# Optimization experiments

Measured on AMD Instinct MI355X. Metric: run time of the kernel, lower is better.

Reference implementation:

```python
import jax, jax.numpy as jnp
import numpy as np

B = 16      # number of point clouds
N = 4096    # points per cloud (max after densify)
D = 3       # xyz


def setup_inputs() -> dict:
    key = jax.random.key(0)
    k1, k2 = jax.random.split(key)
    pred = jax.random.normal(k1, (B * N, D), dtype=jnp.float32)
    target = jax.random.normal(k2, (B * N, D), dtype=jnp.float32)
    # sorted segment ids, equal-sized clouds (faithful to to_dense_batch usage)
    batch = jnp.repeat(jnp.arange(B, dtype=jnp.int64), N)
    return {"pred": pred, "target": target, "batch": batch}


def to_dense_batch(x, batch, num_batches, max_n):
    # PyG to_dense_batch: scatter flat points into [B, max_n, D], zero-padded.
    ones = jnp.ones_like(batch)
    counts = jax.ops.segment_sum(ones, batch, num_segments=num_batches)
    offsets = jnp.concatenate([jnp.zeros((1,), batch.dtype), jnp.cumsum(counts)[:-1]])
    pos = jnp.arange(batch.shape[0], dtype=batch.dtype) - offsets[batch]
    dense = jnp.zeros((num_batches, max_n, x.shape[-1]), x.dtype)
    return dense.at[batch, pos].set(x)


def chamfer_distance(x, y):
    # squared-euclidean pairwise distances via the GEMM identity
    x2 = jnp.sum(x * x, axis=-1)                      # [B, N]
    y2 = jnp.sum(y * y, axis=-1)                      # [B, M]
    xy = jnp.einsum('bnd,bmd->bnm', x, y)             # [B, N, M]
    d = x2[:, :, None] + y2[:, None, :] - 2.0 * xy    # [B, N, M]
    cham_x = jnp.mean(jnp.min(d, axis=2), axis=1)     # mean over N of min over M
    cham_y = jnp.mean(jnp.min(d, axis=1), axis=1)     # mean over M of min over N
    # point_reduction='mean', batch_reduction='mean' (pytorch3d defaults)
    return jnp.mean(cham_x + cham_y)


def reference(pred, target, batch):
    x = to_dense_batch(pred, batch, B, N)
    y = to_dense_batch(target, batch, B, N)
    return chamfer_distance(x, y)
```

## Files before the change

kernel.cpp:

```cpp
#include <hip/hip_runtime.h>


namespace {

constexpr int kB = 16;
constexpr int kN = 4096;
constexpr int kPlane = kB * kN;
constexpr int kStage = 512;
constexpr int kNS = kN / kStage;
constexpr float kScale = 1.0f / (float)(kB * kN);

typedef short bf16x8 __attribute__((ext_vector_type(8)));
typedef float f32x16 __attribute__((ext_vector_type(16)));
typedef unsigned short u16;

__device__ inline u16 bf16_rn(float f) {
  union { float f; unsigned u; } v; v.f = f;
  unsigned r = v.u + 0x7fffu + ((v.u >> 16) & 1u);
  return (u16)(r >> 16);
}
__device__ inline float bf16_f(u16 h) {
  union { unsigned u; float f; } v; v.u = (unsigned)h << 16;
  return v.f;
}
__device__ inline unsigned pk2(u16 lo, u16 hi) {
  return (unsigned)lo | ((unsigned)hi << 16);
}

__global__ void init_out(float* out) { out[0] = 0.0f; }

__global__ __launch_bounds__(256) void cd_prep(
    const float* __restrict__ pred, const float* __restrict__ targ,
    u16* __restrict__ Apred, u16* __restrict__ Atarg,
    u16* __restrict__ Bpred, u16* __restrict__ Btarg,
    float* __restrict__ out) {
  const int p = blockIdx.x * 256 + threadIdx.x;
  if (p == 0) out[0] = 0.0f;
  const int cloud = p >> 12, q = p & (kN - 1);
  const int stg = q >> 9, pl = q & (kStage - 1);
  const size_t boff = (size_t)cloud * 65536 + (size_t)stg * 8192 + (size_t)pl * 8;
  const u16 one = 0x3F80;

  const float* srcs[2] = {pred, targ};
  u16* adsts[2] = {Apred, Atarg};
  u16* bdsts[2] = {Bpred, Btarg};
#pragma unroll
  for (int which = 0; which < 2; ++which) {
    const float a = srcs[which][3 * p], c = srcs[which][3 * p + 1],
                d = srcs[which][3 * p + 2];
    const u16 ah = bf16_rn(a), ch = bf16_rn(c), dh = bf16_rn(d);
    const u16 al = bf16_rn(a - bf16_f(ah));
    const u16 cl = bf16_rn(c - bf16_f(ch));
    const u16 dl = bf16_rn(d - bf16_f(dh));
    const float s2 = fmaf(a, a, fmaf(c, c, d * d));
    const u16 s2h = bf16_rn(s2);
    const u16 s2l = bf16_rn(s2 - bf16_f(s2h));
    {
      uint4 w0, w1;
      w0.x = pk2(ah, ch); w0.y = pk2(dh, al); w0.z = pk2(cl, dl); w0.w = pk2(ah, ch);
      w1.x = pk2(dh, s2h); w1.y = pk2(s2l, one); w1.z = pk2(one, al); w1.w = pk2(cl, dl);
      uint4* dst = reinterpret_cast<uint4*>(adsts[which] + (size_t)p * 16);
      dst[0] = w0; dst[1] = w1;
    }
    {
      const u16 nah = bf16_rn(-2.0f * bf16_f(ah));
      const u16 nch = bf16_rn(-2.0f * bf16_f(ch));
      const u16 ndh = bf16_rn(-2.0f * bf16_f(dh));
      const u16 nal = bf16_rn(-2.0f * bf16_f(al));
      const u16 ncl = bf16_rn(-2.0f * bf16_f(cl));
      const u16 ndl = bf16_rn(-2.0f * bf16_f(dl));
      uint4 w0, w1;
      w0.x = pk2(nah, nch); w0.y = pk2(ndh, nah); w0.z = pk2(nch, ndh); w0.w = pk2(nal, ncl);
      w1.x = pk2(ndl, one); w1.y = pk2(one, s2h); w1.z = pk2(s2l, nal); w1.w = pk2(ncl, ndl);
      *reinterpret_cast<uint4*>(bdsts[which] + boff) = w0;
      *reinterpret_cast<uint4*>(bdsts[which] + boff + 4096) = w1;
    }
  }
}

__global__ __launch_bounds__(256) void cd_mfma(
    const u16* __restrict__ Apred, const u16* __restrict__ Atarg,
    const u16* __restrict__ Bpred, const u16* __restrict__ Btarg,
    float* __restrict__ out) {
  __shared__ uint4 Blds4[2048];
  __shared__ float wsum[4];

  const int t = threadIdx.x;
  const int w = t >> 6, lane = t & 63;
  const int half = lane >> 5, l31 = lane & 31;
  const int chunk = blockIdx.x;
  const int cloud = blockIdx.y;
  const int dir = blockIdx.z;
  const u16* __restrict__ A = dir ? Atarg : Apred;
  const u16* __restrict__ B = dir ? Bpred : Btarg;

  const int arow = cloud * kN + chunk * 128 + w * 32 + l31;
  union { uint4 u; bf16x8 v; } afu;
  afu.u = *reinterpret_cast<const uint4*>(A + (size_t)arow * 16 + half * 8);
  const bf16x8 afrag = afu.v;

  const char* bcloud = (const char*)B + (size_t)cloud * 131072;
  char* ldsbase = (char*)Blds4;
#define STAGE(st, buf)                                                        \
  {                                                                           \
    const char* _src = bcloud + (size_t)(st) * 16384;                         \
    char* _dst = ldsbase + (buf) * 16384;                                     \
    _Pragma("unroll")                                                         \
    for (int i = 0; i < 4; ++i) {                                             \
      __builtin_amdgcn_global_load_lds(                                       \
          (const __attribute__((address_space(1))) void*)(_src +              \
              ((w * 4 + i) * 64 + lane) * 16),                                \
          (__attribute__((address_space(3))) void*)(_dst + (w * 4 + i) * 1024),\
          16, 0, 0);                                                          \
    }                                                                         \
  }

  f32x16 zacc;
#pragma unroll
  for (int r = 0; r < 16; ++r) zacc[r] = 0.0f;
  float rmin[16];
#pragma unroll
  for (int r = 0; r < 16; ++r) rmin[r] = 1e30f;

  STAGE(0, 0);
  __syncthreads();

  for (int st = 0; st < kNS; ++st) {
    if (st < kNS - 1) STAGE(st + 1, (st + 1) & 1);
    const char* blc = ldsbase + (st & 1) * 16384 + half * 8192 + l31 * 16;
#pragma unroll
    for (int jt = 0; jt < kStage / 64; ++jt) {
      union { uint4 u; bf16x8 v; } B0, B1;
      B0.u = *reinterpret_cast<const uint4*>(blc + jt * 1024);
      B1.u = *reinterpret_cast<const uint4*>(blc + jt * 1024 + 512);
      const f32x16 s0 =
          __builtin_amdgcn_mfma_f32_32x32x16_bf16(afrag, B0.v, zacc, 0, 0, 0);
      const f32x16 s1 =
          __builtin_amdgcn_mfma_f32_32x32x16_bf16(afrag, B1.v, zacc, 0, 0, 0);
#pragma unroll
      for (int r = 0; r < 16; ++r)
        asm("v_min3_f32 %0, %0, %1, %2"
            : "+v"(rmin[r]) : "v"(s0[r]), "v"(s1[r]));
    }
    __syncthreads();
  }
#undef STAGE

#pragma unroll
  for (int st = 1; st < 32; st <<= 1) {
#pragma unroll
    for (int r = 0; r < 16; ++r)
      rmin[r] = fminf(rmin[r], __shfl_xor(rmin[r], st, 64));
  }
  float s = 0.0f;
#pragma unroll
  for (int r = 0; r < 16; ++r) s += rmin[r];
  s = (l31 == 0) ? s : 0.0f;
  s += __shfl_down(s, 32, 64);
  if (lane == 0) wsum[w] = s;
  __syncthreads();
  if (t == 0)
    atomicAdd(out, (wsum[0] + wsum[1] + wsum[2] + wsum[3]) * kScale);
}

template <int KX>
__global__ __launch_bounds__(256) void chamfer_direct(
    const float* __restrict__ pred, const float* __restrict__ targ,
    float* __restrict__ out) {
  __shared__ float4 tA[128], tB[128];
  const int t = threadIdx.x;
  const int xb = blockIdx.x, b = blockIdx.y, dir = blockIdx.z;
  const float* __restrict__ X = dir ? targ : pred;
  const float* __restrict__ Y = dir ? pred : targ;
  float2 xx2[KX], xy2[KX], xz2[KX];
  float x2[KX], mn[KX];
  const int ibase = b * kN + xb * (256 * KX) + t;
#pragma unroll
  for (int k = 0; k < KX; ++k) {
    const int i = ibase + k * 256;
    const float a = X[3 * i], c = X[3 * i + 1], d = X[3 * i + 2];
    x2[k] = fmaf(a, a, fmaf(c, c, d * d));
    xx2[k] = make_float2(-2.0f * a, -2.0f * a);
    xy2[k] = make_float2(-2.0f * c, -2.0f * c);
    xz2[k] = make_float2(-2.0f * d, -2.0f * d);
    mn[k] = 1e30f;
  }
  for (int t0 = 0; t0 < kN; t0 += 256) {
    __syncthreads();
    if (t < 128) {
      const int j0 = 3 * (b * kN + t0 + 2 * t);
      const float a0 = Y[j0], c0 = Y[j0 + 1], d0 = Y[j0 + 2];
      const float a1 = Y[j0 + 3], c1 = Y[j0 + 4], d1 = Y[j0 + 5];
      tA[t] = make_float4(a0, a1, c0, c1);
      tB[t] = make_float4(d0, d1, fmaf(a0, a0, fmaf(c0, c0, d0 * d0)),
                          fmaf(a1, a1, fmaf(c1, c1, d1 * d1)));
    }
    __syncthreads();
    for (int jj = 0; jj < 128; ++jj) {
      const float4 qa = tA[jj], qb = tB[jj];
      const float2 qx = make_float2(qa.x, qa.y), qy = make_float2(qa.z, qa.w);
      const float2 qz = make_float2(qb.x, qb.y), qw = make_float2(qb.z, qb.w);
#pragma unroll
      for (int k = 0; k < KX; ++k) {
        float2 acc;
        asm("v_pk_fma_f32 %0, %1, %2, %3\n\t"
            "v_pk_fma_f32 %0, %4, %5, %0\n\t"
            "v_pk_fma_f32 %0, %6, %7, %0"
            : "=&v"(acc)
            : "v"(xz2[k]), "v"(qz), "v"(qw), "v"(xy2[k]), "v"(qy),
              "v"(xx2[k]), "v"(qx));
        asm("v_min3_f32 %0, %0, %1, %2" : "+v"(mn[k]) : "v"(acc.x), "v"(acc.y));
      }
    }
  }
  float s = 0.0f;
#pragma unroll
  for (int k = 0; k < KX; ++k) s += x2[k] + mn[k];
  for (int o = 32; o > 0; o >>= 1) s += __shfl_down(s, o, 64);
  __shared__ float wsum[4];
  const int lane = t & 63, wv = t >> 6;
  if (lane == 0) wsum[wv] = s;
  __syncthreads();
  if (t == 0)
    atomicAdd(out, (wsum[0] + wsum[1] + wsum[2] + wsum[3]) * kScale);
}

}

extern "C" void kernel_launch(void* const* d_in, const int* in_sizes, int n_in,
                              void* d_out, int out_size, void* d_ws,
                              size_t ws_size, hipStream_t stream) {
  const float* pred = (const float*)d_in[0];
  const float* targ = (const float*)d_in[1];
  float* out = (float*)d_out;

  const size_t needOne = (size_t)kPlane * 16 * sizeof(u16);
  if (ws_size >= 4 * needOne) {
    u16* Apred = (u16*)d_ws;
    u16* Atarg = (u16*)((char*)d_ws + needOne);
    u16* Bpred = (u16*)((char*)d_ws + 2 * needOne);
    u16* Btarg = (u16*)((char*)d_ws + 3 * needOne);
    cd_prep<<<dim3(kPlane / 256), 256, 0, stream>>>(pred, targ, Apred, Atarg,
                                                    Bpred, Btarg, out);
    cd_mfma<<<dim3(32, kB, 2), 256, 0, stream>>>(Apred, Atarg, Bpred, Btarg,
                                                 out);
  } else {
    init_out<<<dim3(1), dim3(1), 0, stream>>>(out);
    constexpr int KX = 8;
    dim3 grid(kN / (256 * KX), kB, 2);
    chamfer_direct<KX><<<grid, 256, 0, stream>>>(pred, targ, out);
  }
}
```

Measured before the change: 94.92 us.

## Switch chamfer MFMA from 32x32x16 to 16x16x32 with half-lane K packing

Replaces the 32x32x16 bf16 MFMA tiles with 16x16x32 tiles. The A and B fragment packing is reordered so the split-bf16 K=16 operand occupies only two lane groups, and the other two groups are fed zeros from a padded LDS slot. Each wave now issues two MFMAs per 16 target columns against two 16-row A fragments, and the min reduction shrinks to four-element accumulators with smaller shuffle trees. The aim is cheaper min work per MFMA output and fewer accumulator registers. The cost is that half the lanes carry zero K data, so more MFMA instructions are issued for the same number of distances.

```diff
diff --git a/kernel.cpp b/kernel.cpp
--- a/kernel.cpp
+++ b/kernel.cpp
@@ -11,7 +11,7 @@
 constexpr float kScale = 1.0f / (float)(kB * kN);
 
 typedef short bf16x8 __attribute__((ext_vector_type(8)));
-typedef float f32x16 __attribute__((ext_vector_type(16)));
+typedef float f32x4 __attribute__((ext_vector_type(4)));
 typedef unsigned short u16;
 
 __device__ inline u16 bf16_rn(float f) {
@@ -58,7 +58,7 @@
     {
       uint4 w0, w1;
       w0.x = pk2(ah, ch); w0.y = pk2(dh, al); w0.z = pk2(cl, dl); w0.w = pk2(ah, ch);
-      w1.x = pk2(dh, s2h); w1.y = pk2(s2l, one); w1.z = pk2(one, al); w1.w = pk2(cl, dl);
+      w1.x = pk2(dh, al); w1.y = pk2(cl, dl); w1.z = pk2(s2h, s2l); w1.w = pk2(one, one);
       uint4* dst = reinterpret_cast<uint4*>(adsts[which] + (size_t)p * 16);
       dst[0] = w0; dst[1] = w1;
     }
@@ -71,7 +71,7 @@
       const u16 ndl = bf16_rn(-2.0f * bf16_f(dl));
       uint4 w0, w1;
       w0.x = pk2(nah, nch); w0.y = pk2(ndh, nah); w0.z = pk2(nch, ndh); w0.w = pk2(nal, ncl);
-      w1.x = pk2(ndl, one); w1.y = pk2(one, s2h); w1.z = pk2(s2l, nal); w1.w = pk2(ncl, ndl);
+      w1.x = pk2(ndl, nal); w1.y = pk2(ncl, ndl); w1.z = pk2(one, one); w1.w = pk2(s2h, s2l);
       *reinterpret_cast<uint4*>(bdsts[which] + boff) = w0;
       *reinterpret_cast<uint4*>(bdsts[which] + boff + 4096) = w1;
     }
@@ -82,22 +82,28 @@
     const u16* __restrict__ Apred, const u16* __restrict__ Atarg,
     const u16* __restrict__ Bpred, const u16* __restrict__ Btarg,
     float* __restrict__ out) {
-  __shared__ uint4 Blds4[2048];
+  __shared__ uint4 Blds4[2052];
   __shared__ float wsum[4];
 
   const int t = threadIdx.x;
   const int w = t >> 6, lane = t & 63;
-  const int half = lane >> 5, l31 = lane & 31;
+  const int l15 = lane & 15, kg = lane >> 4;
+  const bool act = (kg < 2);
+  const int g = kg & 1;
   const int chunk = blockIdx.x;
   const int cloud = blockIdx.y;
   const int dir = blockIdx.z;
   const u16* __restrict__ A = dir ? Atarg : Apred;
   const u16* __restrict__ B = dir ? Bpred : Btarg;
 
-  const int arow = cloud * kN + chunk * 128 + w * 32 + l31;
-  union { uint4 u; bf16x8 v; } afu;
-  afu.u = *reinterpret_cast<const uint4*>(A + (size_t)arow * 16 + half * 8);
-  const bf16x8 afrag = afu.v;
+  const int arow0 = cloud * kN + chunk * 128 + w * 32 + l15;
+  union { uint4 u; bf16x8 v; } af0, af1;
+  af0.u = make_uint4(0, 0, 0, 0);
+  af1.u = make_uint4(0, 0, 0, 0);
+  if (act) {
+    af0.u = *reinterpret_cast<const uint4*>(A + (size_t)arow0 * 16 + g * 8);
+    af1.u = *reinterpret_cast<const uint4*>(A + (size_t)(arow0 + 16) * 16 + g * 8);
+  }
 
   const char* bcloud = (const char*)B + (size_t)cloud * 131072;
   char* ldsbase = (char*)Blds4;
@@ -115,48 +121,57 @@
     }                                                                         \
   }
 
-  f32x16 zacc;
-#pragma unroll
-  for (int r = 0; r < 16; ++r) zacc[r] = 0.0f;
-  float rmin[16];
-#pragma unroll
-  for (int r = 0; r < 16; ++r) rmin[r] = 1e30f;
+  const int rb0 = act ? (g * 8192 + l15 * 16) : 32768;
+  const int rstep = act ? 256 : 0;
+  const int bufstep = act ? 16384 : 0;
+
+  f32x4 z4;
+#pragma unroll
+  for (int r = 0; r < 4; ++r) z4[r] = 0.0f;
+  float rmin0[4], rmin1[4];
+#pragma unroll
+  for (int r = 0; r < 4; ++r) { rmin0[r] = 1e30f; rmin1[r] = 1e30f; }
 
   STAGE(0, 0);
+  if (t == 0) Blds4[2048] = make_uint4(0, 0, 0, 0);
   __syncthreads();
 
   for (int st = 0; st < kNS; ++st) {
     if (st < kNS - 1) STAGE(st + 1, (st + 1) & 1);
-    const char* blc = ldsbase + (st & 1) * 16384 + half * 8192 + l31 * 16;
-#pragma unroll
-    for (int jt = 0; jt < kStage / 64; ++jt) {
-      union { uint4 u; bf16x8 v; } B0, B1;
-      B0.u = *reinterpret_cast<const uint4*>(blc + jt * 1024);
-      B1.u = *reinterpret_cast<const uint4*>(blc + jt * 1024 + 512);
-      const f32x16 s0 =
-          __builtin_amdgcn_mfma_f32_32x32x16_bf16(afrag, B0.v, zacc, 0, 0, 0);
-      const f32x16 s1 =
-          __builtin_amdgcn_mfma_f32_32x32x16_bf16(afrag, B1.v, zacc, 0, 0, 0);
-#pragma unroll
-      for (int r = 0; r < 16; ++r)
-        asm("v_min3_f32 %0, %0, %1, %2"
-            : "+v"(rmin[r]) : "v"(s0[r]), "v"(s1[r]));
+    const char* pb = ldsbase + rb0 + (st & 1) * bufstep;
+#pragma unroll 4
+    for (int jt = 0; jt < kStage / 16; ++jt) {
+      union { uint4 u; bf16x8 v; } bu;
+      bu.u = *reinterpret_cast<const uint4*>(pb);
+      pb += rstep;
+      const f32x4 s0 =
+          __builtin_amdgcn_mfma_f32_16x16x32_bf16(af0.v, bu.v, z4, 0, 0, 0);
+      const f32x4 s1 =
+          __builtin_amdgcn_mfma_f32_16x16x32_bf16(af1.v, bu.v, z4, 0, 0, 0);
+#pragma unroll
+      for (int r = 0; r < 4; ++r) {
+        rmin0[r] = fminf(rmin0[r], s0[r]);
+        rmin1[r] = fminf(rmin1[r], s1[r]);
+      }
     }
     __syncthreads();
   }
 #undef STAGE
 
 #pragma unroll
-  for (int st = 1; st < 32; st <<= 1) {
-#pragma unroll
-    for (int r = 0; r < 16; ++r)
-      rmin[r] = fminf(rmin[r], __shfl_xor(rmin[r], st, 64));
+  for (int sh = 1; sh < 16; sh <<= 1) {
+#pragma unroll
+    for (int r = 0; r < 4; ++r) {
+      rmin0[r] = fminf(rmin0[r], __shfl_xor(rmin0[r], sh, 64));
+      rmin1[r] = fminf(rmin1[r], __shfl_xor(rmin1[r], sh, 64));
+    }
   }
   float s = 0.0f;
 #pragma unroll
-  for (int r = 0; r < 16; ++r) s += rmin[r];
-  s = (l31 == 0) ? s : 0.0f;
-  s += __shfl_down(s, 32, 64);
+  for (int r = 0; r < 4; ++r) s += rmin0[r] + rmin1[r];
+  s = (l15 == 0) ? s : 0.0f;
+  s += __shfl_xor(s, 16, 64);
+  s += __shfl_xor(s, 32, 64);
   if (lane == 0) wsum[w] = s;
   __syncthreads();
   if (t == 0)
```

New measurement: 100.5 us. 1.06x slower.
